# Kernel optimization log

Measured on AMD Instinct MI355X. Metric: run time of the kernel, lower is better.

Reference implementation:

```python
import jax, jax.numpy as jnp
import numpy as np

H = 8          # num heads
HD = 64        # head dim
DV = 512       # values_dim
DC = 128       # coords_dim
DI = 512       # att_inner_dim
DF = 2048      # mlp inner dim


def _ln(x, g, b, eps=1e-5):
    mu = jnp.mean(x, -1, keepdims=True)
    var = jnp.mean((x - mu) ** 2, -1, keepdims=True)
    return (x - mu) * jax.lax.rsqrt(var + eps) * g + b


def _rms(x, g, eps=1e-6):
    return x * jax.lax.rsqrt(jnp.mean(x * x, -1, keepdims=True) + eps) * g


def _heads(x):  # b n (h d) -> b h n d
    b, n, _ = x.shape
    return x.reshape(b, n, H, HD).transpose(0, 2, 1, 3)


def setup_inputs() -> dict:
    key = jax.random.key(0)
    ks = iter(jax.random.split(key, 40))
    r = lambda shape, s=0.02: jax.random.normal(next(ks), shape, jnp.float32) * s
    inp = {
        'coords': jax.random.normal(next(ks), (4, 4096, DC), jnp.float32),
        'values': jax.random.normal(next(ks), (4, 4096, DV), jnp.float32),
        'Lv': jax.random.normal(next(ks), (4, 1024, DV), jnp.float32),
        'Lc': jax.random.normal(next(ks), (4, 1024, DC), jnp.float32),
        'lam': jax.random.normal(next(ks), (1,), jnp.float32),
        'lvn_g': jnp.ones((DV,)), 'lvn_b': jnp.zeros((DV,)),
        'lcn_g': jnp.ones((DC,)), 'lcn_b': jnp.zeros((DC,)),
        'ck_w': r((DC, DI)), 'ck_b': jnp.zeros((DI,)), 'ck_g': jnp.ones((DI,)),
        'cq_w': r((DC, DI)), 'cq_b': jnp.zeros((DI,)), 'cq_g': jnp.ones((DI,)),
        'vq_w': r((DV, DI)), 'vq_b': jnp.zeros((DI,)), 'vq_g': jnp.ones((DI,)),
        'vk_w': r((DV, 2 * DI)), 'vk_b': jnp.zeros((2 * DI,)),
        'op_w': r((DI, DV)), 'op_b': jnp.zeros((DV,)),
        'oln_g': jnp.ones((DV,)), 'oln_b': jnp.zeros((DV,)),
        'm1_w': r((DV, DF)), 'm1_b': jnp.zeros((DF,)),
        'm2_w': r((DF, DF)), 'm2_b': jnp.zeros((DF,)),
        'm3_w': r((DF, DV)), 'm3_b': jnp.zeros((DV,)),
    }
    return inp


def reference(coords, values, Lv, Lc, lam, lvn_g, lvn_b, lcn_g, lcn_b,
              ck_w, ck_b, ck_g, cq_w, cq_b, cq_g, vq_w, vq_b, vq_g,
              vk_w, vk_b, op_w, op_b, oln_g, oln_b,
              m1_w, m1_b, m2_w, m2_b, m3_w, m3_b):
    Lv = _ln(Lv, lvn_g, lvn_b)
    Lc = _ln(Lc, lcn_g, lcn_b)
    vk = Lv @ vk_w + vk_b                     # [b, nl, 2*DI]
    v_v, k_v = jnp.split(vk, 2, axis=-1)
    k_c = _rms(Lc @ ck_w + ck_b, ck_g)
    k_c, v_v, k_v = _heads(k_c), _heads(v_v), _heads(k_v)  # [b,h,nl,d]
    q_v = _heads(_rms(values @ vq_w + vq_b, vq_g))         # [b,h,nq,d]
    q_c = _heads(_rms(coords @ cq_w + cq_b, cq_g))
    # dual-score attention
    scores = jnp.einsum('bhnd,bhmd->bhnm', q_c, k_c) \
        + lam[0] * jnp.einsum('bhnd,bhmd->bhnm', q_v, k_v)
    scores = scores / np.float32(np.sqrt(HD))
    attn = jax.nn.softmax(scores, axis=-1)
    V_out = jnp.einsum('bhnm,bhmd->bhnd', attn, v_v)       # [b,h,nq,d]
    b, _, nq, _ = V_out.shape
    V_out = V_out.transpose(0, 2, 1, 3).reshape(b, nq, DI)
    V_out = V_out @ op_w + op_b
    # (LayerNorm, MLP) head: Linear-GELU-Linear-GELU-Linear
    h = _ln(V_out, oln_g, oln_b)
    h = jax.nn.gelu(h @ m1_w + m1_b)
    h = jax.nn.gelu(h @ m2_w + m2_b)
    return h @ m3_w + m3_b
```

## Files before the change

### kernel.cpp

```cpp
#include <hip/hip_runtime.h>
#include <cstdint>
#include <cstddef>

typedef __bf16 bf16_t;
typedef __bf16 bf16x8 __attribute__((ext_vector_type(8)));
typedef __bf16 bf16x4 __attribute__((ext_vector_type(4)));
typedef __bf16 bf16x2 __attribute__((ext_vector_type(2)));
typedef float  f32x4  __attribute__((ext_vector_type(4)));

typedef __attribute__((address_space(1))) void gvoid_t;
typedef __attribute__((address_space(3))) void lvoid_t;

__device__ __forceinline__ f32x4 mfma16(bf16x8 a, bf16x8 b, f32x4 c) {
  return __builtin_amdgcn_mfma_f32_16x16x32_bf16(a, b, c, 0, 0, 0);
}

__device__ __forceinline__ void async_copy16(const void* g, void* l) {
  __builtin_amdgcn_global_load_lds((gvoid_t*)g, (lvoid_t*)l, 16, 0, 0);
}

__device__ __forceinline__ float gelu_tanh(float x) {
  float u = 0.7978845608028654f * (x + 0.044715f * x * x * x);
  float e = exp2f(2.8853900817779268f * u);
  float t = 1.f - 2.f / (e + 1.f);
  return 0.5f * x * (1.f + t);
}

struct TransBatch {
  const float* src[8];
  bf16_t* dst[8];
  int K[8], N[8], bx[8], base[8];
};

__global__ void transpose_batch_kernel(TransBatch d) {
  int id = blockIdx.x;
  int mi = 0;
#pragma unroll
  for (int j = 1; j < 8; j++)
    if (id >= d.base[j]) mi = j;
  int local = id - d.base[mi];
  int bxw = d.bx[mi];
  int n0 = (local % bxw) * 32, k0 = (local / bxw) * 32;
  const float* in = d.src[mi];
  bf16_t* out = d.dst[mi];
  int K = d.K[mi], N = d.N[mi];

  __shared__ float t[32][33];
  int tx = threadIdx.x, ty = threadIdx.y;
#pragma unroll
  for (int i = 0; i < 4; i++)
    t[ty + i * 8][tx] = in[(size_t)(k0 + ty + i * 8) * N + n0 + tx];
  __syncthreads();
#pragma unroll
  for (int i = 0; i < 4; i++)
    out[(size_t)(n0 + ty + i * 8) * K + k0 + tx] = (bf16_t)t[tx][ty + i * 8];
}

__global__ void transpose_v_kernel(const bf16_t* __restrict__ vk, bf16_t* __restrict__ vt) {
  __shared__ bf16_t t[32][33];
  int b = blockIdx.z;
  int d0 = blockIdx.x * 32, m0 = blockIdx.y * 32;
  int tx = threadIdx.x, ty = threadIdx.y;
#pragma unroll
  for (int i = 0; i < 4; i++)
    t[ty + i * 8][tx] = vk[((size_t)b * 1024 + m0 + ty + i * 8) * 1024 + d0 + tx];
  __syncthreads();
#pragma unroll
  for (int i = 0; i < 4; i++)
    vt[((size_t)b * 512 + d0 + ty + i * 8) * 1024 + m0 + tx] = t[tx][ty + i * 8];
}

__global__ void cvt2_bf16_kernel(const float* __restrict__ a, bf16_t* __restrict__ oa, int n4a,
                                 const float* __restrict__ b, bf16_t* __restrict__ ob, int n4b) {
  int i = blockIdx.x * blockDim.x + threadIdx.x;
  const float* s;
  bf16_t* o;
  int j;
  if (i < n4a) { s = a; o = oa; j = i; }
  else { j = i - n4a; if (j >= n4b) return; s = b; o = ob; }
  float4 v = ((const float4*)s)[j];
  bf16x4 r = {(bf16_t)v.x, (bf16_t)v.y, (bf16_t)v.z, (bf16_t)v.w};
  ((bf16x4*)o)[j] = r;
}

template <int D, bool IS_RMS, typename TI>
__global__ __launch_bounds__(256) void rownorm_kernel(
    const TI* __restrict__ x, const float* __restrict__ g,
    const float* __restrict__ bb, bf16_t* __restrict__ out) {
  constexpr int V = D / 64;
  const int row = blockIdx.x * 4 + (threadIdx.x >> 6);
  const int lane = threadIdx.x & 63;
  const size_t base = (size_t)row * D + (size_t)lane * V;
  float v[V];
  if constexpr (sizeof(TI) == 2) {
    bf16x8 xv = *(const bf16x8*)(x + base);
#pragma unroll
    for (int j = 0; j < V; j++) v[j] = (float)xv[j];
  } else if constexpr (V == 8) {
    float4 a = ((const float4*)(x + base))[0];
    float4 b2 = ((const float4*)(x + base))[1];
    v[0] = a.x; v[1] = a.y; v[2] = a.z; v[3] = a.w;
    v[4] = b2.x; v[5] = b2.y; v[6] = b2.z; v[7] = b2.w;
  } else {
    float2 a = *(const float2*)(x + base);
    v[0] = a.x; v[1] = a.y;
  }
  float s = 0.f, s2 = 0.f;
#pragma unroll
  for (int j = 0; j < V; j++) { s += v[j]; s2 += v[j] * v[j]; }
#pragma unroll
  for (int o = 32; o > 0; o >>= 1) { s += __shfl_xor(s, o); s2 += __shfl_xor(s2, o); }
  float mu, rr;
  if constexpr (IS_RMS) {
    mu = 0.f;
    rr = rsqrtf(s2 * (1.f / D) + 1e-6f);
  } else {
    mu = s * (1.f / D);
    rr = rsqrtf(s2 * (1.f / D) - mu * mu + 1e-5f);
  }
  float o[V];
#pragma unroll
  for (int j = 0; j < V; j++) {
    float gv = g[lane * V + j];
    float bv;
    if constexpr (IS_RMS) bv = 0.f; else bv = bb[lane * V + j];
    o[j] = (v[j] - mu) * rr * gv + bv;
  }
  if constexpr (V == 8) {
    bf16x8 ov;
#pragma unroll
    for (int j = 0; j < 8; j++) ov[j] = (bf16_t)o[j];
    *(bf16x8*)(out + base) = ov;
  } else {
    bf16x2 ov;
    ov[0] = (bf16_t)o[0]; ov[1] = (bf16_t)o[1];
    *(bf16x2*)(out + base) = ov;
  }
}

template <int EPI>
__global__ __launch_bounds__(256, 2) void gemm_bt(
    const bf16_t* __restrict__ A, const bf16_t* __restrict__ Bt,
    const float* __restrict__ bias, void* __restrict__ outp,
    int M, int N, int K) {
  __shared__ __align__(16) bf16_t As[128 * 64];
  __shared__ __align__(16) bf16_t Bs[128 * 64];
  const int tid = threadIdx.x;
  const int lane = tid & 63, wv = tid >> 6;
  const int quad = lane >> 4, l16 = lane & 15;
  int nwg = gridDim.x * gridDim.y;
  int bid = blockIdx.y * gridDim.x + blockIdx.x;
  if (!(nwg & 7)) { int cpx = nwg >> 3; bid = (bid & 7) * cpx + (bid >> 3); }
  const int m_base = (bid / gridDim.x) * 128, n_base = (bid % gridDim.x) * 128;
  const int wm = wv & 1, wn = wv >> 1;
  f32x4 acc[4][4] = {};

  for (int k0 = 0; k0 < K; k0 += 64) {
#pragma unroll
    for (int c = 0; c < 4; c++) {
      int p = c * 256 + tid;
      int row = p >> 3;
      int gc = (p & 7) ^ (row & 7);
      async_copy16(&A[(size_t)(m_base + row) * K + k0 + gc * 8], &As[(size_t)p * 8]);
      async_copy16(&Bt[(size_t)(n_base + row) * K + k0 + gc * 8], &Bs[(size_t)p * 8]);
    }
    __syncthreads();
#pragma unroll
    for (int ks = 0; ks < 2; ks++) {
      bf16x8 af[4], bfr[4];
#pragma unroll
      for (int mi = 0; mi < 4; mi++) {
        int r = wm * 64 + mi * 16 + l16;
        int c = (ks * 4 + quad) ^ (r & 7);
        af[mi] = *(const bf16x8*)&As[(size_t)(r * 8 + c) * 8];
      }
#pragma unroll
      for (int ni = 0; ni < 4; ni++) {
        int r = wn * 64 + ni * 16 + l16;
        int c = (ks * 4 + quad) ^ (r & 7);
        bfr[ni] = *(const bf16x8*)&Bs[(size_t)(r * 8 + c) * 8];
      }
#pragma unroll
      for (int mi = 0; mi < 4; mi++)
#pragma unroll
        for (int ni = 0; ni < 4; ni++)
          acc[mi][ni] = mfma16(af[mi], bfr[ni], acc[mi][ni]);
    }
    __syncthreads();
  }

#pragma unroll
  for (int mi = 0; mi < 4; mi++) {
    int m = m_base + wm * 64 + mi * 16 + quad * 4;
#pragma unroll
    for (int ni = 0; ni < 4; ni++) {
      int n = n_base + wn * 64 + ni * 16 + l16;
      float bv = bias[n];
#pragma unroll
      for (int r2 = 0; r2 < 4; r2++) {
        float v = acc[mi][ni][r2] + bv;
        if (EPI == 2) v = gelu_tanh(v);
        if (EPI == 0) ((float*)outp)[(size_t)(m + r2) * N + n] = v;
        else          ((bf16_t*)outp)[(size_t)(m + r2) * N + n] = (bf16_t)v;
      }
    }
  }
}

#define SCHED_FENCE() __builtin_amdgcn_sched_barrier(0)

#define PH_TAIL(...) \
  SCHED_FENCE(); \
  __builtin_amdgcn_s_barrier(); \
  asm volatile("s_waitcnt lgkmcnt(0)" ::: "memory"); \
  SCHED_FENCE(); \
  __builtin_amdgcn_s_setprio(1); \
  __VA_ARGS__; \
  __builtin_amdgcn_s_setprio(0); \
  SCHED_FENCE(); \
  __builtin_amdgcn_s_barrier();

#define PH_TAIL_VM(...) \
  asm volatile("s_waitcnt vmcnt(6)" ::: "memory"); \
  PH_TAIL(__VA_ARGS__)

#define LGKM_DRAIN8() asm volatile("s_waitcnt lgkmcnt(8)" ::: "memory")

template <int EPI>
__global__ __launch_bounds__(512, 2) void gemm256(
    const bf16_t* __restrict__ A, const bf16_t* __restrict__ Bt,
    const float* __restrict__ bias, void* __restrict__ outp,
    int M, int N, int K) {
  __shared__ __align__(16) bf16_t As[2][256 * 64];
  __shared__ __align__(16) bf16_t Bs[2][256 * 64];
  const int tid = threadIdx.x;
  const int lane = tid & 63, wid = tid >> 6;
  const int quad = lane >> 4, l16 = lane & 15;
  const int wm = wid >> 2, wn = wid & 3;
  int nwg = gridDim.x * gridDim.y;
  int bid = blockIdx.y * gridDim.x + blockIdx.x;
  if (!(nwg & 7)) { int cpx = nwg >> 3; bid = (bid & 7) * cpx + (bid >> 3); }
  const int m_base = (bid / gridDim.x) * 256, n_base = (bid % gridDim.x) * 256;
  const int nkt = K >> 6, nit = nkt >> 1;

  f32x4 acc[8][4] = {};

  auto stA = [&](int buf, int half, int kt) {
    if (kt >= nkt) kt = 0;
    const bf16_t* src = A + (size_t)(m_base + half * 128) * K + kt * 64;
    bf16_t* dst = &As[buf][half * 128 * 64];
#pragma unroll
    for (int i = 0; i < 2; i++) {
      int p = i * 512 + tid;
      int r = p >> 3, pc = p & 7;
      int gc = pc ^ (r & 7);
      async_copy16(&src[(size_t)r * K + gc * 8], &dst[(size_t)p * 8]);
    }
  };
  auto stB = [&](int buf, int half, int kt) {
    if (kt >= nkt) kt = 0;
    const bf16_t* src = Bt + (size_t)(n_base + half * 128) * K + kt * 64;
    bf16_t* dst = &Bs[buf][half * 128 * 64];
#pragma unroll
    for (int i = 0; i < 2; i++) {
      int p = i * 512 + tid;
      int r = p >> 3, pc = p & 7;
      int gc = pc ^ (r & 7);
      async_copy16(&src[(size_t)r * K + gc * 8], &dst[(size_t)p * 8]);
    }
  };
  auto ldA = [&](const bf16_t* Asb, int rg, bf16x8 (&af)[2][2]) {
#pragma unroll
    for (int mi = 0; mi < 2; mi++) {
      int r = wm * 128 + rg * 32 + mi * 16 + l16;
#pragma unroll
      for (int ks = 0; ks < 2; ks++) {
        int c = (ks * 4 + quad) ^ (r & 7);
        af[mi][ks] = *(const bf16x8*)&Asb[(size_t)(r * 8 + c) * 8];
      }
    }
  };
  auto ldB = [&](const bf16_t* Bsb, bf16x8 (&bfr)[4][2]) {
#pragma unroll
    for (int cf = 0; cf < 4; cf++) {
      int r = wn * 64 + cf * 16 + l16;
#pragma unroll
      for (int ks = 0; ks < 2; ks++) {
        int c = (ks * 4 + quad) ^ (r & 7);
        bfr[cf][ks] = *(const bf16x8*)&Bsb[(size_t)(r * 8 + c) * 8];
      }
    }
  };
  auto mm = [&](int rg, bf16x8 (&a)[2][2], bf16x8 (&b)[4][2]) {
#pragma unroll
    for (int ks = 0; ks < 2; ks++)
#pragma unroll
      for (int mi = 0; mi < 2; mi++)
#pragma unroll
        for (int cf = 0; cf < 4; cf++)
          acc[rg * 2 + mi][cf] = mfma16(a[mi][ks], b[cf][ks], acc[rg * 2 + mi][cf]);
  };

  stB(0, 0, 0); stB(0, 1, 0); stA(0, 0, 0); stA(0, 1, 0);
  stB(1, 0, 1); stB(1, 1, 1); stA(1, 0, 1);
  asm volatile("s_waitcnt vmcnt(6)" ::: "memory");
  SCHED_FENCE();
  __builtin_amdgcn_s_barrier();

  bf16x8 af[2][2], afn[2][2], bfr[4][2];
  for (int it = 0; it < nit; ++it) {
    const int O = 2 * it + 1, F = 2 * it + 2, G = 2 * it + 3;
    ldB(Bs[0], bfr); ldA(As[0], 0, af);
    stA(1, 1, O);
    LGKM_DRAIN8();
    PH_TAIL(mm(0, af, bfr));
    ldA(As[0], 1, af);
    stB(0, 0, F);
    PH_TAIL(mm(1, af, bfr));
    ldA(As[0], 2, af); ldA(As[0], 3, afn);
    stB(0, 1, F);
    PH_TAIL(mm(2, af, bfr));
    stA(0, 0, F);
    PH_TAIL_VM(mm(3, afn, bfr));
    ldB(Bs[1], bfr); ldA(As[1], 0, af);
    stA(0, 1, F);
    LGKM_DRAIN8();
    PH_TAIL(mm(0, af, bfr));
    ldA(As[1], 1, af);
    stB(1, 0, G);
    PH_TAIL(mm(1, af, bfr));
    ldA(As[1], 2, af); ldA(As[1], 3, afn);
    stB(1, 1, G);
    PH_TAIL(mm(2, af, bfr));
    stA(1, 0, G);
    PH_TAIL_VM(mm(3, afn, bfr));
  }
  asm volatile("s_waitcnt vmcnt(0)" ::: "memory");

#pragma unroll
  for (int rf = 0; rf < 8; rf++) {
    int m = m_base + wm * 128 + rf * 16 + quad * 4;
#pragma unroll
    for (int cf = 0; cf < 4; cf++) {
      int n = n_base + wn * 64 + cf * 16 + l16;
      float bv = bias[n];
#pragma unroll
      for (int r2 = 0; r2 < 4; r2++) {
        float v = acc[rf][cf][r2] + bv;
        if (EPI == 2) v = gelu_tanh(v);
        if (EPI == 0) ((float*)outp)[(size_t)(m + r2) * N + n] = v;
        else          ((bf16_t*)outp)[(size_t)(m + r2) * N + n] = (bf16_t)v;
      }
    }
  }
}

template <int EPI>
__global__ __launch_bounds__(256, 2) void gemm64(
    const bf16_t* __restrict__ A, const bf16_t* __restrict__ Bt,
    const float* __restrict__ bias, void* __restrict__ outp,
    int M, int N, int K) {
  __shared__ __align__(16) bf16_t As[64 * 32];
  __shared__ __align__(16) bf16_t Bs[128 * 32];
  const int tid = threadIdx.x;
  const int lane = tid & 63, wv = tid >> 6;
  const int quad = lane >> 4, l16 = lane & 15;
  const int m_base = blockIdx.y * 64, n_base = blockIdx.x * 128;
  const int wm = wv & 1, wn = wv >> 1;
  f32x4 acc[2][4] = {};

  for (int k0 = 0; k0 < K; k0 += 32) {
    {
      int p = tid;
      int row = p >> 2;
      int kc = (p & 3) ^ ((row >> 1) & 3);
      async_copy16(&A[(size_t)(m_base + row) * K + k0 + kc * 8], &As[(size_t)p * 8]);
    }
#pragma unroll
    for (int c = 0; c < 2; c++) {
      int p = c * 256 + tid;
      int row = p >> 2;
      int kc = (p & 3) ^ ((row >> 1) & 3);
      async_copy16(&Bt[(size_t)(n_base + row) * K + k0 + kc * 8], &Bs[(size_t)p * 8]);
    }
    __syncthreads();
    bf16x8 af[2], bfr[4];
#pragma unroll
    for (int mi = 0; mi < 2; mi++) {
      int r = wm * 32 + mi * 16 + l16;
      int kc = quad ^ ((r >> 1) & 3);
      af[mi] = *(const bf16x8*)&As[(size_t)(r * 4 + kc) * 8];
    }
#pragma unroll
    for (int ni = 0; ni < 4; ni++) {
      int r = wn * 64 + ni * 16 + l16;
      int kc = quad ^ ((r >> 1) & 3);
      bfr[ni] = *(const bf16x8*)&Bs[(size_t)(r * 4 + kc) * 8];
    }
#pragma unroll
    for (int mi = 0; mi < 2; mi++)
#pragma unroll
      for (int ni = 0; ni < 4; ni++)
        acc[mi][ni] = mfma16(af[mi], bfr[ni], acc[mi][ni]);
    __syncthreads();
  }

#pragma unroll
  for (int mi = 0; mi < 2; mi++) {
    int m = m_base + wm * 32 + mi * 16 + quad * 4;
#pragma unroll
    for (int ni = 0; ni < 4; ni++) {
      int n = n_base + wn * 64 + ni * 16 + l16;
      float bv = bias[n];
#pragma unroll
      for (int r2 = 0; r2 < 4; r2++) {
        float v = acc[mi][ni][r2] + bv;
        if (EPI == 2) v = gelu_tanh(v);
        if (EPI == 0) ((float*)outp)[(size_t)(m + r2) * N + n] = v;
        else          ((bf16_t*)outp)[(size_t)(m + r2) * N + n] = (bf16_t)v;
      }
    }
  }
}

__global__ __launch_bounds__(256, 2) void attn_kernel(
    const bf16_t* __restrict__ qc, const bf16_t* __restrict__ qv,
    const bf16_t* __restrict__ kcb, const bf16_t* __restrict__ vkb,
    const bf16_t* __restrict__ vt, const float* __restrict__ lamp,
    bf16_t* __restrict__ vout) {
  const int b = blockIdx.z, h = blockIdx.y;
  const int tid = threadIdx.x;
  const int lane = tid & 63, wv = tid >> 6;
  const int quad = lane >> 4, l16 = lane & 15;
  const int qrow0 = blockIdx.x * 128 + wv * 32;
  const float SCL = 0.125f * 1.4426950408889634f;
  const float C1 = SCL, C2 = lamp[0] * SCL;

  __shared__ __align__(16) bf16_t kcS[64 * 64];
  __shared__ __align__(16) bf16_t kvS[64 * 64];
  __shared__ __align__(16) bf16_t vtS[64 * 64];
  __shared__ __align__(16) bf16_t sP[4][32 * 64];
  bf16_t* sPw = sP[wv];

  bf16x8 qcf[2][2], qvf[2][2];
#pragma unroll
  for (int mt = 0; mt < 2; mt++)
#pragma unroll
    for (int ks = 0; ks < 2; ks++) {
      size_t o = ((size_t)b * 4096 + qrow0 + mt * 16 + l16) * 512 + h * 64 + ks * 32 + quad * 8;
      qcf[mt][ks] = *(const bf16x8*)&qc[o];
      qvf[mt][ks] = *(const bf16x8*)&qv[o];
    }

  f32x4 O[2][4] = {};
  float ls[2][4] = {};

  for (int kb = 0; kb < 16; kb++) {
#pragma unroll
    for (int i = 0; i < 2; i++) {
      int p = i * 256 + tid;
      int row = p >> 3;
      int gc = (p & 7) ^ (row & 7);
      async_copy16(&kcb[((size_t)b * 1024 + kb * 64 + row) * 512 + h * 64 + gc * 8],
                   &kcS[(size_t)p * 8]);
      async_copy16(&vkb[((size_t)b * 1024 + kb * 64 + row) * 1024 + 512 + h * 64 + gc * 8],
                   &kvS[(size_t)p * 8]);
      async_copy16(&vt[((size_t)((b * 8 + h) * 64) + row) * 1024 + kb * 64 + gc * 8],
                   &vtS[(size_t)p * 8]);
    }
    __syncthreads();

#pragma unroll
    for (int nt = 0; nt < 4; nt++) {
      int krow = nt * 16 + l16;
      int kb8 = krow & 7;
      bf16x8 kc0 = *(const bf16x8*)&kcS[(size_t)(krow * 8 + (quad ^ kb8)) * 8];
      bf16x8 kc1 = *(const bf16x8*)&kcS[(size_t)(krow * 8 + ((4 + quad) ^ kb8)) * 8];
      bf16x8 kv0 = *(const bf16x8*)&kvS[(size_t)(krow * 8 + (quad ^ kb8)) * 8];
      bf16x8 kv1 = *(const bf16x8*)&kvS[(size_t)(krow * 8 + ((4 + quad) ^ kb8)) * 8];
#pragma unroll
      for (int mt = 0; mt < 2; mt++) {
        f32x4 sc = {};
        sc = mfma16(qcf[mt][0], kc0, sc);
        sc = mfma16(qcf[mt][1], kc1, sc);
        f32x4 sv = {};
        sv = mfma16(qvf[mt][0], kv0, sv);
        sv = mfma16(qvf[mt][1], kv1, sv);
#pragma unroll
        for (int r = 0; r < 4; r++) {
          float p = exp2f(sc[r] * C1 + sv[r] * C2);
          ls[mt][r] += p;
          int prow = mt * 16 + quad * 4 + r;
          int col = nt * 16 + l16;
          sPw[prow * 64 + (((col >> 3) ^ (prow & 7)) * 8) + (col & 7)] = (bf16_t)p;
        }
      }
    }
    asm volatile("s_waitcnt lgkmcnt(0)" ::: "memory");

#pragma unroll
    for (int ks2 = 0; ks2 < 2; ks2++) {
      bf16x8 pa[2];
#pragma unroll
      for (int mt = 0; mt < 2; mt++) {
        int prow = mt * 16 + l16;
        pa[mt] = *(const bf16x8*)&sPw[(size_t)(prow * 8 + ((ks2 * 4 + quad) ^ (prow & 7))) * 8];
      }
#pragma unroll
      for (int ntd = 0; ntd < 4; ntd++) {
        int drow = ntd * 16 + l16;
        bf16x8 vb = *(const bf16x8*)&vtS[(size_t)(drow * 8 + ((ks2 * 4 + quad) ^ (drow & 7))) * 8];
        O[0][ntd] = mfma16(pa[0], vb, O[0][ntd]);
        O[1][ntd] = mfma16(pa[1], vb, O[1][ntd]);
      }
    }
    __syncthreads();
  }

#pragma unroll
  for (int mt = 0; mt < 2; mt++) {
    float inv[4];
#pragma unroll
    for (int r = 0; r < 4; r++) {
      float v = ls[mt][r];
      v += __shfl_xor(v, 1);
      v += __shfl_xor(v, 2);
      v += __shfl_xor(v, 4);
      v += __shfl_xor(v, 8);
      inv[r] = 1.f / v;
    }
#pragma unroll
    for (int ntd = 0; ntd < 4; ntd++)
#pragma unroll
      for (int r = 0; r < 4; r++) {
        size_t o = ((size_t)b * 4096 + qrow0 + mt * 16 + quad * 4 + r) * 512 + h * 64 + ntd * 16 + l16;
        vout[o] = (bf16_t)(O[mt][ntd][r] * inv[r]);
      }
  }
}

extern "C" void kernel_launch(void* const* d_in, const int* in_sizes, int n_in,
                              void* d_out, int out_size, void* d_ws, size_t ws_size,
                              hipStream_t stream) {
  (void)in_sizes; (void)n_in; (void)out_size; (void)ws_size;
  const float* coords = (const float*)d_in[0];
  const float* values = (const float*)d_in[1];
  const float* Lv     = (const float*)d_in[2];
  const float* Lc     = (const float*)d_in[3];
  const float* lam    = (const float*)d_in[4];
  const float* lvn_g  = (const float*)d_in[5];
  const float* lvn_b  = (const float*)d_in[6];
  const float* lcn_g  = (const float*)d_in[7];
  const float* lcn_b  = (const float*)d_in[8];
  const float* ck_w = (const float*)d_in[9];  const float* ck_b = (const float*)d_in[10]; const float* ck_g = (const float*)d_in[11];
  const float* cq_w = (const float*)d_in[12]; const float* cq_b = (const float*)d_in[13]; const float* cq_g = (const float*)d_in[14];
  const float* vq_w = (const float*)d_in[15]; const float* vq_b = (const float*)d_in[16]; const float* vq_g = (const float*)d_in[17];
  const float* vk_w = (const float*)d_in[18]; const float* vk_b = (const float*)d_in[19];
  const float* op_w = (const float*)d_in[20]; const float* op_b = (const float*)d_in[21];
  const float* oln_g = (const float*)d_in[22]; const float* oln_b = (const float*)d_in[23];
  const float* m1_w = (const float*)d_in[24]; const float* m1_b = (const float*)d_in[25];
  const float* m2_w = (const float*)d_in[26]; const float* m2_b = (const float*)d_in[27];
  const float* m3_w = (const float*)d_in[28]; const float* m3_b = (const float*)d_in[29];

  char* ws = (char*)d_ws;
  size_t off = 0;
  auto alloc = [&](size_t bytes) { void* p = ws + off; off += (bytes + 255) & ~(size_t)255; return p; };

  bf16_t* wt_m1 = (bf16_t*)alloc((size_t)512 * 2048 * 2);
  bf16_t* wt_m2 = (bf16_t*)alloc((size_t)2048 * 2048 * 2);
  bf16_t* wt_m3 = (bf16_t*)alloc((size_t)2048 * 512 * 2);
  bf16_t* scr0  = (bf16_t*)alloc((size_t)16384 * 512 * 4);
  bf16_t* qv_bf = (bf16_t*)alloc((size_t)16384 * 512 * 2);
  bf16_t* qc_bf = (bf16_t*)alloc((size_t)16384 * 512 * 2);
  bf16_t* voutb = (bf16_t*)alloc((size_t)16384 * 512 * 2);
  bf16_t* h0    = (bf16_t*)alloc((size_t)16384 * 512 * 2);
  bf16_t* h1    = (bf16_t*)alloc((size_t)16384 * 2048 * 2);
  bf16_t* h2    = (bf16_t*)alloc((size_t)16384 * 2048 * 2);

  size_t ov = (size_t)((char*)h1 - ws);
  auto oalloc = [&](size_t bytes) { void* p = ws + ov; ov += (bytes + 255) & ~(size_t)255; return p; };
  bf16_t* wt_vk = (bf16_t*)oalloc((size_t)1024 * 512 * 2);
  bf16_t* wt_ck = (bf16_t*)oalloc((size_t)512 * 128 * 2);
  bf16_t* wt_cq = (bf16_t*)oalloc((size_t)512 * 128 * 2);
  bf16_t* wt_vq = (bf16_t*)oalloc((size_t)512 * 512 * 2);
  bf16_t* wt_op = (bf16_t*)oalloc((size_t)512 * 512 * 2);
  bf16_t* lv_ln = (bf16_t*)oalloc((size_t)4096 * 512 * 2);
  bf16_t* lc_ln = (bf16_t*)oalloc((size_t)4096 * 128 * 2);
  bf16_t* vkob  = (bf16_t*)oalloc((size_t)4096 * 1024 * 2);
  bf16_t* kc_b  = (bf16_t*)oalloc((size_t)4096 * 512 * 2);
  bf16_t* kc_bf = (bf16_t*)oalloc((size_t)4096 * 512 * 2);
  bf16_t* val_bf= (bf16_t*)oalloc((size_t)16384 * 512 * 2);
  bf16_t* crd_bf= (bf16_t*)oalloc((size_t)16384 * 128 * 2);
  bf16_t* vt    = (bf16_t*)oalloc((size_t)4 * 512 * 1024 * 2);

  TransBatch tb8;
  const float* srcs[8] = {vk_w, ck_w, cq_w, vq_w, op_w, m1_w, m2_w, m3_w};
  bf16_t* dsts[8] = {wt_vk, wt_ck, wt_cq, wt_vq, wt_op, wt_m1, wt_m2, wt_m3};
  int Ks[8] = {512, 128, 128, 512, 512, 512, 2048, 2048};
  int Ns[8] = {1024, 512, 512, 512, 512, 2048, 2048, 512};
  int cum = 0;
  for (int i = 0; i < 8; i++) {
    tb8.src[i] = srcs[i]; tb8.dst[i] = dsts[i];
    tb8.K[i] = Ks[i]; tb8.N[i] = Ns[i];
    tb8.bx[i] = Ns[i] / 32;
    tb8.base[i] = cum;
    cum += (Ns[i] / 32) * (Ks[i] / 32);
  }
  transpose_batch_kernel<<<cum, dim3(32, 8), 0, stream>>>(tb8);

  cvt2_bf16_kernel<<<(16384 * 512 / 4 + 16384 * 128 / 4 + 255) / 256, 256, 0, stream>>>(
      values, val_bf, 16384 * 512 / 4, coords, crd_bf, 16384 * 128 / 4);

  rownorm_kernel<512, false, float><<<1024, 256, 0, stream>>>(Lv, lvn_g, lvn_b, lv_ln);
  rownorm_kernel<128, false, float><<<1024, 256, 0, stream>>>(Lc, lcn_g, lcn_b, lc_ln);

  gemm_bt<1><<<dim3(8, 32), 256, 0, stream>>>(lv_ln, wt_vk, vk_b, vkob, 4096, 1024, 512);
  gemm64<1><<<dim3(4, 64), 256, 0, stream>>>(lc_ln, wt_ck, ck_b, kc_b, 4096, 512, 128);
  rownorm_kernel<512, true, bf16_t><<<1024, 256, 0, stream>>>(kc_b, ck_g, nullptr, kc_bf);

  gemm_bt<1><<<dim3(4, 128), 256, 0, stream>>>(val_bf, wt_vq, vq_b, scr0, 16384, 512, 512);
  rownorm_kernel<512, true, bf16_t><<<4096, 256, 0, stream>>>(scr0, vq_g, nullptr, qv_bf);
  gemm64<1><<<dim3(4, 256), 256, 0, stream>>>(crd_bf, wt_cq, cq_b, scr0, 16384, 512, 128);
  rownorm_kernel<512, true, bf16_t><<<4096, 256, 0, stream>>>(scr0, cq_g, nullptr, qc_bf);

  transpose_v_kernel<<<dim3(16, 32, 4), dim3(32, 8), 0, stream>>>(vkob, vt);

  attn_kernel<<<dim3(32, 8, 4), 256, 0, stream>>>(qc_bf, qv_bf, kc_bf, vkob, vt, lam, voutb);

  gemm_bt<1><<<dim3(4, 128), 256, 0, stream>>>(voutb, wt_op, op_b, scr0, 16384, 512, 512);
  rownorm_kernel<512, false, bf16_t><<<4096, 256, 0, stream>>>(scr0, oln_g, oln_b, h0);

  gemm256<2><<<dim3(8, 64), 512, 0, stream>>>(h0, wt_m1, m1_b, h1, 16384, 2048, 512);
  gemm256<2><<<dim3(8, 64), 512, 0, stream>>>(h1, wt_m2, m2_b, h2, 16384, 2048, 2048);
  gemm_bt<0><<<dim3(4, 128), 256, 0, stream>>>(h2, wt_m3, m3_b, (float*)d_out, 16384, 512, 2048);
}
```

Baseline: 598.9 us.

## Streamline gemm256 pipeline with pointer-incremented staging and single barrier per phase

Rewrites the gemm256 main loop so global-to-LDS staging uses precomputed per-thread source pointers that are bumped each k-tile, and LDS fragment reads use precomputed swizzled base addresses. This removes per-call index arithmetic and the kt wraparound check. Each phase now has one barrier instead of two, and the partial lgkmcnt drains are dropped. The m1 GEMM (K=512) is moved to the smaller-tile gemm_bt kernel. The wraparound removal means the last iterations may prefetch past the matrix end, and dropping a barrier could introduce LDS races if the hazard ordering is wrong.

Result: slower. 646.6 us (+8.0%).

```diff
diff --git a/kernel.cpp b/kernel.cpp
--- a/kernel.cpp
+++ b/kernel.cpp
@@ -209,22 +209,28 @@
 
 #define SCHED_FENCE() __builtin_amdgcn_sched_barrier(0)
 
-#define PH_TAIL(...) \
+#define PHT(MM) \
   SCHED_FENCE(); \
-  __builtin_amdgcn_s_barrier(); \
   asm volatile("s_waitcnt lgkmcnt(0)" ::: "memory"); \
   SCHED_FENCE(); \
   __builtin_amdgcn_s_setprio(1); \
-  __VA_ARGS__; \
+  MM; \
   __builtin_amdgcn_s_setprio(0); \
   SCHED_FENCE(); \
-  __builtin_amdgcn_s_barrier();
-
-#define PH_TAIL_VM(...) \
+  __builtin_amdgcn_s_barrier(); \
+  SCHED_FENCE();
+
+#define PHT_VM(MM) \
+  SCHED_FENCE(); \
+  asm volatile("s_waitcnt lgkmcnt(0)" ::: "memory"); \
+  SCHED_FENCE(); \
+  __builtin_amdgcn_s_setprio(1); \
+  MM; \
+  __builtin_amdgcn_s_setprio(0); \
+  SCHED_FENCE(); \
   asm volatile("s_waitcnt vmcnt(6)" ::: "memory"); \
-  PH_TAIL(__VA_ARGS__)
-
-#define LGKM_DRAIN8() asm volatile("s_waitcnt lgkmcnt(8)" ::: "memory")
+  __builtin_amdgcn_s_barrier(); \
+  SCHED_FENCE();
 
 template <int EPI>
 __global__ __launch_bounds__(512, 2) void gemm256(
@@ -235,7 +241,7 @@
   __shared__ __align__(16) bf16_t Bs[2][256 * 64];
   const int tid = threadIdx.x;
   const int lane = tid & 63, wid = tid >> 6;
-  const int quad = lane >> 4, l16 = lane & 15;
+  const int quad = lane >> 4, l16 = lane & 15, l7 = l16 & 7;
   const int wm = wid >> 2, wn = wid & 3;
   int nwg = gridDim.x * gridDim.y;
   int bid = blockIdx.y * gridDim.x + blockIdx.x;
@@ -245,51 +251,25 @@
 
   f32x4 acc[8][4] = {};
 
-  auto stA = [&](int buf, int half, int kt) {
-    if (kt >= nkt) kt = 0;
-    const bf16_t* src = A + (size_t)(m_base + half * 128) * K + kt * 64;
-    bf16_t* dst = &As[buf][half * 128 * 64];
-#pragma unroll
-    for (int i = 0; i < 2; i++) {
-      int p = i * 512 + tid;
-      int r = p >> 3, pc = p & 7;
-      int gc = pc ^ (r & 7);
-      async_copy16(&src[(size_t)r * K + gc * 8], &dst[(size_t)p * 8]);
-    }
+  const bf16_t* aB[2], * bB[2];
+#pragma unroll
+  for (int ks = 0; ks < 2; ks++) {
+    aB[ks] = &As[0][0] + (wm * 128 + l16) * 64 + (((ks * 4 + quad) ^ l7)) * 8;
+    bB[ks] = &Bs[0][0] + (wn * 64 + l16) * 64 + (((ks * 4 + quad) ^ l7)) * 8;
+  }
+  auto ldA = [&](int buf, int rg, bf16x8 (&af)[2][2]) {
+#pragma unroll
+    for (int mi = 0; mi < 2; mi++)
+#pragma unroll
+      for (int ks = 0; ks < 2; ks++)
+        af[mi][ks] = *(const bf16x8*)(aB[ks] + buf * 16384 + rg * 2048 + mi * 1024);
   };
-  auto stB = [&](int buf, int half, int kt) {
-    if (kt >= nkt) kt = 0;
-    const bf16_t* src = Bt + (size_t)(n_base + half * 128) * K + kt * 64;
-    bf16_t* dst = &Bs[buf][half * 128 * 64];
-#pragma unroll
-    for (int i = 0; i < 2; i++) {
-      int p = i * 512 + tid;
-      int r = p >> 3, pc = p & 7;
-      int gc = pc ^ (r & 7);
-      async_copy16(&src[(size_t)r * K + gc * 8], &dst[(size_t)p * 8]);
-    }
-  };
-  auto ldA = [&](const bf16_t* Asb, int rg, bf16x8 (&af)[2][2]) {
-#pragma unroll
-    for (int mi = 0; mi < 2; mi++) {
-      int r = wm * 128 + rg * 32 + mi * 16 + l16;
-#pragma unroll
-      for (int ks = 0; ks < 2; ks++) {
-        int c = (ks * 4 + quad) ^ (r & 7);
-        af[mi][ks] = *(const bf16x8*)&Asb[(size_t)(r * 8 + c) * 8];
-      }
-    }
-  };
-  auto ldB = [&](const bf16_t* Bsb, bf16x8 (&bfr)[4][2]) {
-#pragma unroll
-    for (int cf = 0; cf < 4; cf++) {
-      int r = wn * 64 + cf * 16 + l16;
-#pragma unroll
-      for (int ks = 0; ks < 2; ks++) {
-        int c = (ks * 4 + quad) ^ (r & 7);
-        bfr[cf][ks] = *(const bf16x8*)&Bsb[(size_t)(r * 8 + c) * 8];
-      }
-    }
+  auto ldB = [&](int buf, bf16x8 (&bfr)[4][2]) {
+#pragma unroll
+    for (int cf = 0; cf < 4; cf++)
+#pragma unroll
+      for (int ks = 0; ks < 2; ks++)
+        bfr[cf][ks] = *(const bf16x8*)(bB[ks] + buf * 16384 + cf * 1024);
   };
   auto mm = [&](int rg, bf16x8 (&a)[2][2], bf16x8 (&b)[4][2]) {
 #pragma unroll
@@ -301,39 +281,60 @@
           acc[rg * 2 + mi][cf] = mfma16(a[mi][ks], b[cf][ks], acc[rg * 2 + mi][cf]);
   };
 
-  stB(0, 0, 0); stB(0, 1, 0); stA(0, 0, 0); stA(0, 1, 0);
-  stB(1, 0, 1); stB(1, 1, 1); stA(1, 0, 1);
+  const int rr = tid >> 3;
+  const int cb = ((tid & 7) ^ (rr & 7)) * 16;
+  const char* pa00 = (const char*)A + 2 * ((size_t)(m_base + 0 + rr) * K) + cb;
+  const char* pa01 = (const char*)A + 2 * ((size_t)(m_base + 64 + rr) * K) + cb;
+  const char* pa10 = (const char*)A + 2 * ((size_t)(m_base + 128 + rr) * K) + cb;
+  const char* pa11 = (const char*)A + 2 * ((size_t)(m_base + 192 + rr) * K) + cb;
+  const char* pb00 = (const char*)Bt + 2 * ((size_t)(n_base + 0 + rr) * K) + cb;
+  const char* pb01 = (const char*)Bt + 2 * ((size_t)(n_base + 64 + rr) * K) + cb;
+  const char* pb10 = (const char*)Bt + 2 * ((size_t)(n_base + 128 + rr) * K) + cb;
+  const char* pb11 = (const char*)Bt + 2 * ((size_t)(n_base + 192 + rr) * K) + cb;
+  bf16_t* dA0 = &As[0][0] + tid * 8;
+  bf16_t* dB0 = &Bs[0][0] + tid * 8;
+  auto stage = [&](const char*& p0, const char*& p1, bf16_t* d0) {
+    async_copy16(p0, d0);
+    async_copy16(p1, d0 + 4096);
+    p0 += 128; p1 += 128;
+  };
+
+  stage(pb00, pb01, dB0);
+  stage(pb10, pb11, dB0 + 8192);
+  stage(pa00, pa01, dA0);
+  stage(pa10, pa11, dA0 + 8192);
+  stage(pb00, pb01, dB0 + 16384);
+  stage(pb10, pb11, dB0 + 16384 + 8192);
+  stage(pa00, pa01, dA0 + 16384);
   asm volatile("s_waitcnt vmcnt(6)" ::: "memory");
   SCHED_FENCE();
   __builtin_amdgcn_s_barrier();
+  SCHED_FENCE();
 
   bf16x8 af[2][2], afn[2][2], bfr[4][2];
   for (int it = 0; it < nit; ++it) {
-    const int O = 2 * it + 1, F = 2 * it + 2, G = 2 * it + 3;
-    ldB(Bs[0], bfr); ldA(As[0], 0, af);
-    stA(1, 1, O);
-    LGKM_DRAIN8();
-    PH_TAIL(mm(0, af, bfr));
-    ldA(As[0], 1, af);
-    stB(0, 0, F);
-    PH_TAIL(mm(1, af, bfr));
-    ldA(As[0], 2, af); ldA(As[0], 3, afn);
-    stB(0, 1, F);
-    PH_TAIL(mm(2, af, bfr));
-    stA(0, 0, F);
-    PH_TAIL_VM(mm(3, afn, bfr));
-    ldB(Bs[1], bfr); ldA(As[1], 0, af);
-    stA(0, 1, F);
-    LGKM_DRAIN8();
-    PH_TAIL(mm(0, af, bfr));
-    ldA(As[1], 1, af);
-    stB(1, 0, G);
-    PH_TAIL(mm(1, af, bfr));
-    ldA(As[1], 2, af); ldA(As[1], 3, afn);
-    stB(1, 1, G);
-    PH_TAIL(mm(2, af, bfr));
-    stA(1, 0, G);
-    PH_TAIL_VM(mm(3, afn, bfr));
+    ldB(0, bfr); ldA(0, 0, af);
+    stage(pa10, pa11, dA0 + 16384 + 8192);
+    PHT(mm(0, af, bfr));
+    ldA(0, 1, af);
+    stage(pb00, pb01, dB0);
+    PHT(mm(1, af, bfr));
+    ldA(0, 2, af); ldA(0, 3, afn);
+    stage(pb10, pb11, dB0 + 8192);
+    PHT(mm(2, af, bfr));
+    stage(pa00, pa01, dA0);
+    PHT_VM(mm(3, afn, bfr));
+    ldB(1, bfr); ldA(1, 0, af);
+    stage(pa10, pa11, dA0 + 8192);
+    PHT(mm(0, af, bfr));
+    ldA(1, 1, af);
+    stage(pb00, pb01, dB0 + 16384);
+    PHT(mm(1, af, bfr));
+    ldA(1, 2, af); ldA(1, 3, afn);
+    stage(pb10, pb11, dB0 + 16384 + 8192);
+    PHT(mm(2, af, bfr));
+    stage(pa00, pa01, dA0 + 16384);
+    PHT_VM(mm(3, afn, bfr));
   }
   asm volatile("s_waitcnt vmcnt(0)" ::: "memory");
 
@@ -630,7 +631,7 @@
   gemm_bt<1><<<dim3(4, 128), 256, 0, stream>>>(voutb, wt_op, op_b, scr0, 16384, 512, 512);
   rownorm_kernel<512, false, bf16_t><<<4096, 256, 0, stream>>>(scr0, oln_g, oln_b, h0);
 
-  gemm256<2><<<dim3(8, 64), 512, 0, stream>>>(h0, wt_m1, m1_b, h1, 16384, 2048, 512);
+  gemm_bt<2><<<dim3(16, 128), 256, 0, stream>>>(h0, wt_m1, m1_b, h1, 16384, 2048, 512);
   gemm256<2><<<dim3(8, 64), 512, 0, stream>>>(h1, wt_m2, m2_b, h2, 16384, 2048, 2048);
   gemm_bt<0><<<dim3(4, 128), 256, 0, stream>>>(h2, wt_m3, m3_b, (float*)d_out, 16384, 512, 2048);
 }
```
